# Kernel optimization log

Hardware: AMD Instinct MI355X
Metric: run time of the kernel (lower is better)

## Reference

```python
import jax, jax.numpy as jnp
import numpy as np

B, HH, WW, E = 8, 64, 64, 384
NH, EXP = 6, 2
D1 = (EXP * E) // NH * NH      # 768
HD = D1 // NH                  # 128
RPE = 512
LAYERS = 3
EPS = 1e-6


def srms(x):
    # SimpleRMSNorm: no learnable weight
    return x * jax.lax.rsqrt(jnp.mean(x * x, axis=-1, keepdims=True) + EPS)


def rpe_forward(pos, pw, pb, lw, lb, ow, ob):
    # pos: (n, 1) -> (n, NH*HD). Rpe MLP: act(pos_proj) -> layers x [norm,act,linear] -> out
    x = jax.nn.relu(pos @ pw + pb)
    for i in range(lw.shape[0]):  # fixed small layer count
        x = jax.nn.relu(srms(x)) @ lw[i] + lb[i]
    return jax.nn.relu(srms(x)) @ ow + ob


def tno_coeffs(n, pw, pb, lw, lb, ow, ob):
    # Toeplitz coeffs t_0..t_{n-1}, t_0(dummy), t_{-(n-1)}..t_{-1} for circular conv of len 2n
    pos = jnp.arange(1, n, dtype=jnp.float32)[:, None]             # (n-1, 1), par_type=1
    neg = -jnp.arange(1, n, dtype=jnp.float32)[::-1][:, None]      # -(n-1)..-1
    zero = jnp.zeros((1, 1), dtype=jnp.float32)
    t_zero = rpe_forward(zero, pw, pb, lw, lb, ow, ob)             # (1, NH*HD)
    t_pos = rpe_forward(pos, pw, pb, lw, lb, ow, ob)               # (n-1, NH*HD)
    t_neg = rpe_forward(neg, pw, pb, lw, lb, ow, ob)
    a = jnp.concatenate([t_zero, t_pos, t_zero, t_neg], axis=0)    # (2n, NH*HD)
    return a.reshape(2 * n, NH, HD).transpose(1, 0, 2)             # (NH, 2n, HD)


def tno_apply(v, a, axis):
    # v: (b, h, H, W, d); FFT-based Toeplitz (circular) mixing along `axis` in {-3, -2}
    n = v.shape[axis]
    a = a[:, :, None, :] if axis == -3 else a[:, None, :, :]
    y = jnp.fft.rfft(v, 2 * n, axis=axis)
    af = jnp.fft.rfft(a, 2 * n, axis=axis)
    out = jnp.fft.irfft(af * y, 2 * n, axis=axis)
    return jax.lax.slice_in_dim(out, 0, n, axis=out.ndim + axis)


def setup_inputs() -> dict:
    key = jax.random.key(0)
    ks = jax.random.split(key, 24)
    s = 0.02
    def rn(k, shape):
        return jax.random.normal(k, shape, dtype=jnp.float32) * s
    inp = {
        "x": jax.random.normal(ks[0], (B, HH, WW, E), dtype=jnp.float32),
        "H": HH, "W": WW,
        "Wu": rn(ks[1], (E, D1)), "bu": jnp.zeros((D1,), jnp.float32),
        "Wv": rn(ks[2], (E, D1)), "bv": jnp.zeros((D1,), jnp.float32),
        "Wo": rn(ks[3], (D1, E)), "bo": jnp.zeros((E,), jnp.float32),
    }
    for t, off in (("r1", 4), ("r2", 10)):
        inp[t + "_pw"] = rn(ks[off], (1, RPE))
        inp[t + "_pb"] = jnp.zeros((RPE,), jnp.float32)
        inp[t + "_lw"] = rn(ks[off + 1], (LAYERS, RPE, RPE))
        inp[t + "_lb"] = jnp.zeros((LAYERS, RPE), jnp.float32)
        inp[t + "_ow"] = rn(ks[off + 2], (RPE, NH * HD))
        inp[t + "_ob"] = jnp.zeros((NH * HD,), jnp.float32)
    return inp


def reference(x, H, W, Wu, bu, Wv, bv, Wo, bo,
              r1_pw, r1_pb, r1_lw, r1_lb, r1_ow, r1_ob,
              r2_pw, r2_pb, r2_lw, r2_lb, r2_ow, r2_ob):
    b = x.shape[0]
    xn = srms(x)                                    # pre_norm (SimpleRMSNorm)
    u = jax.nn.silu(xn @ Wu + bu)                   # gate branch
    v = jax.nn.silu(xn @ Wv + bv)
    v = v.reshape(b, H, W, NH, HD).transpose(0, 3, 1, 2, 4)        # b h H W d
    a_h = tno_coeffs(H, r2_pw, r2_pb, r2_lw, r2_lb, r2_ow, r2_ob)  # toep2, dim=-3
    a_w = tno_coeffs(W, r1_pw, r1_pb, r1_lw, r1_lb, r1_ow, r1_ob)  # toep1, dim=-2
    out = tno_apply(v, a_h, -3) + tno_apply(v, a_w, -2)
    out = out.transpose(0, 2, 3, 1, 4).reshape(b, H, W, NH * HD)   # b H W (h d)
    out = u * out
    return out @ Wo + bo + x
```

## Files before the change

### kernel.cpp

```cpp
#include <hip/hip_runtime.h>
#include <stdint.h>


typedef __attribute__((ext_vector_type(4))) float  f32x4;
typedef __attribute__((ext_vector_type(8))) short  s16x8;
typedef __attribute__((ext_vector_type(8))) unsigned short u16x8;
typedef __attribute__((ext_vector_type(4))) unsigned short u16x4;
typedef unsigned short u16;

#define M_TOT 32768
#define E_DIM 384
#define D1    768

__device__ __forceinline__ u16 f2bf(float f) {
  union { float f; unsigned int u; } v; v.f = f;
  unsigned int r = (v.u + 0x7FFFu + ((v.u >> 16) & 1u)) >> 16;
  return (u16)r;
}
__device__ __forceinline__ float bf2f(u16 h) {
  union { unsigned int u; float f; } v; v.u = ((unsigned int)h) << 16;
  return v.f;
}
__device__ __forceinline__ float silu_f(float x) {
  return x * __builtin_amdgcn_rcpf(1.f + __expf(-x));
}

__device__ __forceinline__ void gload_lds16(const u16* g, u16* l) {
  __builtin_amdgcn_global_load_lds(
      (const __attribute__((address_space(1))) uint32_t*)g,
      (__attribute__((address_space(3))) uint32_t*)l, 16, 0, 0);
}

__global__ __launch_bounds__(256) void setup_k(
    const float* __restrict__ x, u16* __restrict__ xn,
    const float* __restrict__ Wu, const float* __restrict__ Wv,
    const float* __restrict__ Wo, u16* __restrict__ Wuvt, u16* __restrict__ Wot,
    const float* __restrict__ r1lw, const float* __restrict__ r1ow,
    const float* __restrict__ r2lw, const float* __restrict__ r2ow,
    u16* __restrict__ lwT, u16* __restrict__ owT,
    const float* __restrict__ r1pw, const float* __restrict__ r1pb,
    const float* __restrict__ r2pw, const float* __restrict__ r2pb,
    float* __restrict__ X0) {
  __shared__ float sm[32][33];
  const int bid = blockIdx.x;
  const int tid = threadIdx.x;

  if (bid < 8192) {
    int row  = bid * 4 + (tid >> 6);
    int lane = tid & 63;
    const float* xr = x + (size_t)row * 384 + lane;
    float v[6]; float ss = 0.f;
#pragma unroll
    for (int i = 0; i < 6; i++) { v[i] = xr[i * 64]; ss += v[i] * v[i]; }
#pragma unroll
    for (int off = 32; off > 0; off >>= 1) ss += __shfl_xor(ss, off);
    float sc = rsqrtf(ss * (1.f / 384.f) + 1e-6f);
    u16* o = xn + (size_t)row * 384 + lane;
#pragma unroll
    for (int i = 0; i < 6; i++) o[i * 64] = f2bf(v[i] * sc);
  } else if (bid < 11360) {
    int b = bid - 8192;
    const float* src; u16* dst; int C, DS, R0, C0;
    if (b < 2304) {
      int mlp = b / 1152, r = b % 1152;
      if (r < 768) {
        int L = r / 256, t = r % 256;
        R0 = (t / 16) * 32; C0 = (t % 16) * 32;
        src = (mlp ? r2lw : r1lw) + (size_t)L * 262144;
        dst = lwT + (size_t)(mlp * 3 + L) * 262144;
        C = 512; DS = 512;
      } else {
        int t = r - 768;
        R0 = (t / 24) * 32; C0 = (t % 24) * 32;
        src = mlp ? r2ow : r1ow;
        dst = owT + (size_t)mlp * 393216;
        C = 768; DS = 512;
      }
    } else {
      int t = b - 2304;
      if (t < 288)      { R0 = (t / 24) * 32; C0 = (t % 24) * 32;
                          src = Wu; C = 768; dst = Wuvt;            DS = 384; }
      else if (t < 576) { int t2 = t - 288; R0 = (t2 / 24) * 32; C0 = (t2 % 24) * 32;
                          src = Wv; C = 768; dst = Wuvt + 768 * 384; DS = 384; }
      else              { int t2 = t - 576; R0 = (t2 / 12) * 32; C0 = (t2 % 12) * 32;
                          src = Wo; C = 384; dst = Wot;             DS = 768; }
    }
    int lx = tid % 32, ly = tid / 32;
#pragma unroll
    for (int q = 0; q < 4; q++) {
      int y = q * 8 + ly;
      sm[y][lx] = src[(size_t)(R0 + y) * C + C0 + lx];
    }
    __syncthreads();
#pragma unroll
    for (int q = 0; q < 4; q++) {
      int y = q * 8 + ly;
      dst[(size_t)(C0 + y) * DS + R0 + lx] = f2bf(sm[lx][y]);
    }
  } else {
    int idx = (bid - 11360) * 256 + tid;
    int gid = idx * 4;
    int row = gid >> 9, col = gid & 511;
    int mlp = row >> 7, p = row & 127;
    float pos = (p < 64) ? (float)p : ((p == 64) ? 0.f : (float)(p - 128));
    const float* pw = (mlp ? r2pw : r1pw) + col;
    const float* pb = (mlp ? r2pb : r1pb) + col;
    f32x4 w = *(const f32x4*)pw;
    f32x4 bb = *(const f32x4*)pb;
    f32x4 o;
#pragma unroll
    for (int e = 0; e < 4; e++) o[e] = fmaxf(pos * w[e] + bb[e], 0.f);
    *(f32x4*)(X0 + gid) = o;
  }
}

template <int N, bool TOUT>
__global__ __launch_bounds__(256) void rpe_layer_k(
    const float* __restrict__ X,
    const u16* __restrict__ wtA, const u16* __restrict__ wtB,
    const float* __restrict__ bA, const float* __restrict__ bB,
    float* __restrict__ outA, float* __restrict__ outB) {
  constexpr int NT = N / 128;
  const int mlp = blockIdx.x / NT;
  const int n0  = (blockIdx.x % NT) * 128;
  const u16* WT = mlp ? wtB : wtA;
  const float* bias = mlp ? bB : bA;
  float* out = mlp ? outB : outA;
  const float* Xm = X + (size_t)mlp * 128 * 512;

  __shared__ float scale[128];
  __shared__ __align__(16) u16 As[128 * 64];
  __shared__ __align__(16) u16 Bs[128 * 64];

  const int tid  = threadIdx.x;
  const int lane = tid & 63;
  const int wid  = tid >> 6;
  const int wm   = wid >> 1, wn = wid & 1;
  const int fl   = lane & 15, fh = lane >> 4;

  {
    int row = tid >> 1, half = tid & 1;
    const float* xr = Xm + (size_t)row * 512 + half * 256;
    float ss = 0.f;
#pragma unroll 8
    for (int q = 0; q < 64; q++) {
      f32x4 v = *(const f32x4*)(xr + q * 4);
      ss += v[0] * v[0] + v[1] * v[1] + v[2] * v[2] + v[3] * v[3];
    }
    ss += __shfl_xor(ss, 1);
    if (!half) scale[row] = rsqrtf(ss * (1.f / 512.f) + 1e-6f);
  }
  __syncthreads();

  f32x4 acc[4][4];
  {
    f32x4 z = {0.f, 0.f, 0.f, 0.f};
#pragma unroll
    for (int i = 0; i < 4; i++)
#pragma unroll
      for (int j = 0; j < 4; j++) acc[i][j] = z;
  }

  const int arow = tid >> 1, acb = (tid & 1) * 32;
  const int sr = tid >> 3, sc = (tid & 7) * 8;

  for (int kt = 0; kt < 512; kt += 64) {
    {
      const float* xp = Xm + (size_t)arow * 512 + kt + acb;
      float s_ = scale[arow];
      u16* dst = As + arow * 64 + acb;
#pragma unroll
      for (int q = 0; q < 8; q++) {
        f32x4 v = *(const f32x4*)(xp + q * 4);
        u16x4 pk;
#pragma unroll
        for (int e = 0; e < 4; e++) pk[e] = f2bf(fmaxf(v[e], 0.f) * s_);
        *(u16x4*)(dst + q * 4) = pk;
      }
    }
    {
      const u16* gB = WT + (size_t)(n0 + sr) * 512 + kt + sc;
      u16* lB = Bs + sr * 64 + sc;
#pragma unroll
      for (int i = 0; i < 4; i++)
        gload_lds16(gB + (size_t)(i * 32) * 512, lB + i * 32 * 64);
    }
    __syncthreads();
#pragma unroll
    for (int ks = 0; ks < 2; ks++) {
      s16x8 af[4], bfr[4];
      const u16* ap = As + (wm * 64 + fl) * 64 + ks * 32 + fh * 8;
      const u16* bp = Bs + (wn * 64 + fl) * 64 + ks * 32 + fh * 8;
#pragma unroll
      for (int i = 0; i < 4; i++) af[i] = *(const s16x8*)(ap + i * 16 * 64);
#pragma unroll
      for (int j = 0; j < 4; j++) bfr[j] = *(const s16x8*)(bp + j * 16 * 64);
#pragma unroll
      for (int i = 0; i < 4; i++)
#pragma unroll
        for (int j = 0; j < 4; j++)
          acc[i][j] = __builtin_amdgcn_mfma_f32_16x16x32_bf16(af[i], bfr[j], acc[i][j], 0, 0, 0);
    }
    __syncthreads();
  }

#pragma unroll
  for (int i = 0; i < 4; i++)
#pragma unroll
    for (int j = 0; j < 4; j++) {
      int c = n0 + wn * 64 + j * 16 + fl;
      float bv_ = bias[c];
#pragma unroll
      for (int q = 0; q < 4; q++) {
        int r = wm * 64 + i * 16 + fh * 4 + q;
        if (TOUT) out[(size_t)c * 128 + r] = acc[i][j][q] + bv_;
        else      out[(size_t)r * N + c]   = acc[i][j][q] + bv_;
      }
    }
}

template <int MODE>
__global__ __launch_bounds__(256) void gemm_k(
    const u16* __restrict__ A, const u16* __restrict__ Bt, int K,
    u16* __restrict__ u_out, u16* __restrict__ vt_out,
    const float* __restrict__ bu, const float* __restrict__ bv,
    float* __restrict__ out, const float* __restrict__ bo,
    const float* __restrict__ xres) {
  __shared__ __align__(16) char smem[34816];
  u16*   As  = (u16*)smem;
  u16*   Bs  = As + 128 * 64;
  float* epi = (float*)smem;

  const int tid  = threadIdx.x;
  const int lane = tid & 63;
  const int wid  = tid >> 6;
  const int wm   = wid >> 1, wn = wid & 1;
  const int bm   = blockIdx.x & 255, bn = blockIdx.x >> 8;
  const int m0   = bm * 128, n0 = bn * 128;
  const int fl   = lane & 15, fh = lane >> 4;

  f32x4 acc[4][4];
  {
    f32x4 z = {0.f, 0.f, 0.f, 0.f};
#pragma unroll
    for (int i = 0; i < 4; i++)
#pragma unroll
      for (int j = 0; j < 4; j++) acc[i][j] = z;
  }

  const int sr  = tid >> 3;
  const int scl = (tid & 7) * 8;
  const int scs = ((tid & 7) ^ (sr & 7)) * 8;
  const int cr  = tid & 63;
  const int mw  = ((tid >> 6) & 3) * 32;

  for (int kt = 0; kt < K; kt += 64) {
    if (MODE == 1) {
      const u16* ga = A + (size_t)(kt + cr) * M_TOT + m0 + mw;
      u16x8 rr[4];
      rr[0] = *(const u16x8*)(ga);
      rr[1] = *(const u16x8*)(ga + 8);
      rr[2] = *(const u16x8*)(ga + 16);
      rr[3] = *(const u16x8*)(ga + 24);
      const int cb8 = cr >> 3, off = cr & 7;
#pragma unroll
      for (int v = 0; v < 4; v++)
#pragma unroll
        for (int e = 0; e < 8; e++)
          As[(mw + v * 8 + e) * 64 + ((cb8 ^ e) << 3) + off] = rr[v][e];
    } else {
      const u16* gA = A + (size_t)(m0 + sr) * K + kt + scs;
      u16* lA = As + sr * 64 + scl;
#pragma unroll
      for (int i = 0; i < 4; i++)
        gload_lds16(gA + (size_t)(i * 32) * K, lA + i * 32 * 64);
    }
    {
      const u16* gB = Bt + (size_t)(n0 + sr) * K + kt + scs;
      u16* lB = Bs + sr * 64 + scl;
#pragma unroll
      for (int i = 0; i < 4; i++)
        gload_lds16(gB + (size_t)(i * 32) * K, lB + i * 32 * 64);
    }
    __syncthreads();
#pragma unroll
    for (int ks = 0; ks < 2; ks++) {
      s16x8 af[4], bfr[4];
      const int xc = ((ks * 4 + fh) ^ (fl & 7)) * 8;
      const u16* ap = As + (wm * 64 + fl) * 64 + xc;
      const u16* bp = Bs + (wn * 64 + fl) * 64 + xc;
#pragma unroll
      for (int i = 0; i < 4; i++) af[i] = *(const s16x8*)(ap + i * 16 * 64);
#pragma unroll
      for (int j = 0; j < 4; j++) bfr[j] = *(const s16x8*)(bp + j * 16 * 64);
#pragma unroll
      for (int i = 0; i < 4; i++)
#pragma unroll
        for (int j = 0; j < 4; j++)
          acc[i][j] = __builtin_amdgcn_mfma_f32_16x16x32_bf16(af[i], bfr[j], acc[i][j], 0, 0, 0);
    }
    __syncthreads();
  }

  for (int half = 0; half < 2; half++) {
    __syncthreads();
    if (wm == half) {
#pragma unroll
      for (int i = 0; i < 4; i++)
#pragma unroll
        for (int j = 0; j < 4; j++) {
          int er = i * 16 + fh * 4;
          int ec = wn * 64 + j * 16 + fl;
#pragma unroll
          for (int q = 0; q < 4; q++) epi[(er + q) * 132 + ec] = acc[i][j][q];
        }
    }
    __syncthreads();
    if (MODE == 0) {
      const bool isU = (n0 < 768);
      u16* baseo = isU ? u_out : vt_out;
      const int cc = tid >> 1;
      const int cg = (isU ? n0 : n0 - 768) + cc;
      const float bias_v = (isU ? bu : bv)[cg];
      u16* dst = baseo + (size_t)cg * M_TOT + m0 + half * 64;
#pragma unroll
      for (int q = 0; q < 4; q++) {
        int mb = (tid & 1) * 8 + q * 16;
        u16x8 pk;
#pragma unroll
        for (int e = 0; e < 8; e++) {
          int mm = mb + e;
          pk[e] = f2bf(silu_f(epi[mm * 132 + cc] + bias_v));
        }
        *(u16x8*)(dst + mb) = pk;
      }
    } else {
      int rr = tid >> 2;
      int gm = m0 + half * 64 + rr;
      const float* xr = xres + (size_t)gm * 384 + n0;
      float* orow = out + (size_t)gm * 384 + n0;
#pragma unroll
      for (int q = 0; q < 8; q++) {
        int cb = (tid & 3) * 4 + q * 16;
        f32x4 xv = *(const f32x4*)(xr + cb);
        f32x4 ov;
#pragma unroll
        for (int e = 0; e < 4; e++) {
          int c = cb + e;
          ov[e] = epi[rr * 132 + c] + bo[n0 + c] + xv[e];
        }
        *(f32x4*)(orow + cb) = ov;
      }
    }
  }
}

__global__ __launch_bounds__(256) void conv_k(const u16* __restrict__ vt,
                                              const u16* __restrict__ ut,
                                              const float* __restrict__ a_hT,
                                              const float* __restrict__ a_wT,
                                              u16* __restrict__ gT) {
  __shared__ __align__(16) char smraw[5 * 64 * 72 * 2 + 1024];
  u16* Vs  = (u16*)smraw;
  u16* VTs = Vs + 64 * 72;
  u16* Ths = VTs + 64 * 72;
  u16* Tws = Ths + 64 * 72;
  u16* Us  = Tws + 64 * 72;
  float* ahs = (float*)(Us + 64 * 72);
  float* aws = ahs + 128;
  u16* epi = Ths;

  const int tid = threadIdx.x;
  const int c = blockIdx.x >> 3, b = blockIdx.x & 7;
  const u16* srcv = vt + (size_t)c * M_TOT + b * 4096;
  const u16* srcu = ut + (size_t)c * M_TOT + b * 4096;

  {
    int y = tid >> 2, x0 = (tid & 3) * 16;
    *(u16x8*)(Vs + y * 72 + x0)     = *(const u16x8*)(srcv + y * 64 + x0);
    *(u16x8*)(Vs + y * 72 + x0 + 8) = *(const u16x8*)(srcv + y * 64 + x0 + 8);
    *(u16x8*)(Us + y * 72 + x0)     = *(const u16x8*)(srcu + y * 64 + x0);
    *(u16x8*)(Us + y * 72 + x0 + 8) = *(const u16x8*)(srcu + y * 64 + x0 + 8);
  }
  if (tid < 128) ahs[tid] = a_hT[(size_t)c * 128 + tid];
  else           aws[tid - 128] = a_wT[(size_t)c * 128 + (tid - 128)];
  __syncthreads();

  {
    int y = tid & 63, j0 = (tid >> 6) * 16;
#pragma unroll
    for (int e = 0; e < 16; e++) {
      int j = j0 + e;
      VTs[j * 72 + y] = Vs[y * 72 + j];
      Ths[y * 72 + j] = f2bf(ahs[(y - j) & 127]);
      Tws[y * 72 + j] = f2bf(aws[(y - j) & 127]);
    }
  }
  __syncthreads();

  const int lane = tid & 63, w = tid >> 6;
  const int fl = lane & 15, fh = lane >> 4;
  f32x4 acc[4];
  {
    f32x4 z = {0.f, 0.f, 0.f, 0.f};
#pragma unroll
    for (int i = 0; i < 4; i++) acc[i] = z;
  }

#pragma unroll
  for (int ks = 0; ks < 2; ks++) {
    s16x8 qh = *(const s16x8*)(Ths + (w * 16 + fl) * 72 + ks * 32 + fh * 8);
#pragma unroll
    for (int i = 0; i < 4; i++) {
      s16x8 p = *(const s16x8*)(VTs + (i * 16 + fl) * 72 + ks * 32 + fh * 8);
      acc[i] = __builtin_amdgcn_mfma_f32_16x16x32_bf16(p, qh, acc[i], 0, 0, 0);
    }
    s16x8 qw = *(const s16x8*)(Vs + (w * 16 + fl) * 72 + ks * 32 + fh * 8);
#pragma unroll
    for (int i = 0; i < 4; i++) {
      s16x8 p = *(const s16x8*)(Tws + (i * 16 + fl) * 72 + ks * 32 + fh * 8);
      acc[i] = __builtin_amdgcn_mfma_f32_16x16x32_bf16(p, qw, acc[i], 0, 0, 0);
    }
  }
  __syncthreads();

  {
    int y = w * 16 + fl;
#pragma unroll
    for (int i = 0; i < 4; i++) {
      u16x4 pk;
#pragma unroll
      for (int e = 0; e < 4; e++) {
        int xx = i * 16 + fh * 4 + e;
        pk[e] = f2bf(acc[i][e] * bf2f(Us[y * 72 + xx]));
      }
      *(u16x4*)(epi + y * 72 + i * 16 + fh * 4) = pk;
    }
  }
  __syncthreads();

  {
    int y = tid >> 2, x0 = (tid & 3) * 16;
    u16x8 a0 = *(const u16x8*)(epi + y * 72 + x0);
    u16x8 a1 = *(const u16x8*)(epi + y * 72 + x0 + 8);
    u16* dst = gT + (size_t)c * M_TOT + b * 4096 + y * 64 + x0;
    *(u16x8*)dst = a0;
    *(u16x8*)(dst + 8) = a1;
  }
}

extern "C" void kernel_launch(void* const* d_in, const int* in_sizes, int n_in,
                              void* d_out, int out_size, void* d_ws, size_t ws_size,
                              hipStream_t stream) {
  const float* x    = (const float*)d_in[0];
  const float* Wu   = (const float*)d_in[3];
  const float* bu   = (const float*)d_in[4];
  const float* Wv   = (const float*)d_in[5];
  const float* bv   = (const float*)d_in[6];
  const float* Wo   = (const float*)d_in[7];
  const float* bo   = (const float*)d_in[8];
  const float* r1pw = (const float*)d_in[9];
  const float* r1pb = (const float*)d_in[10];
  const float* r1lw = (const float*)d_in[11];
  const float* r1lb = (const float*)d_in[12];
  const float* r1ow = (const float*)d_in[13];
  const float* r1ob = (const float*)d_in[14];
  const float* r2pw = (const float*)d_in[15];
  const float* r2pb = (const float*)d_in[16];
  const float* r2lw = (const float*)d_in[17];
  const float* r2lb = (const float*)d_in[18];
  const float* r2ow = (const float*)d_in[19];
  const float* r2ob = (const float*)d_in[20];
  float* outp = (float*)d_out;

  char* ws = (char*)d_ws;
  size_t off = 0;
  auto carve = [&](size_t bytes) {
    char* p = ws + off;
    off += (bytes + 255) & ~(size_t)255;
    return p;
  };
  u16*   xn   = (u16*)carve((size_t)M_TOT * 384 * 2);
  u16*   uT   = (u16*)carve((size_t)768 * M_TOT * 2);
  u16*   vT   = (u16*)carve((size_t)768 * M_TOT * 2);
  u16*   gT   = (u16*)carve((size_t)768 * M_TOT * 2);
  u16*   Wuvt = (u16*)carve((size_t)1536 * 384 * 2);
  u16*   Wot  = (u16*)carve((size_t)384 * 768 * 2);
  float* awT  = (float*)carve((size_t)768 * 128 * 4);
  float* ahT  = (float*)carve((size_t)768 * 128 * 4);

  char* rb  = (char*)gT;
  u16*   lwT = (u16*)rb;
  u16*   owT = (u16*)(rb + 3145728);
  float* X0  = (float*)(rb + 3145728 + 1572864);
  float* X1  = X0 + 256 * 512;

  setup_k<<<11488, 256, 0, stream>>>(x, xn, Wu, Wv, Wo, Wuvt, Wot,
                                     r1lw, r1ow, r2lw, r2ow, lwT, owT,
                                     r1pw, r1pb, r2pw, r2pb, X0);

  rpe_layer_k<512, false><<<8, 256, 0, stream>>>(X0, lwT, lwT + 3 * 262144,
                                                 r1lb, r2lb, X1, X1 + 128 * 512);
  rpe_layer_k<512, false><<<8, 256, 0, stream>>>(X1, lwT + 262144, lwT + 4 * 262144,
                                                 r1lb + 512, r2lb + 512, X0, X0 + 128 * 512);
  rpe_layer_k<512, false><<<8, 256, 0, stream>>>(X0, lwT + 2 * 262144, lwT + 5 * 262144,
                                                 r1lb + 1024, r2lb + 1024, X1, X1 + 128 * 512);
  rpe_layer_k<768, true><<<12, 256, 0, stream>>>(X1, owT, owT + 393216,
                                                 r1ob, r2ob, awT, ahT);

  gemm_k<0><<<256 * 12, 256, 0, stream>>>(xn, Wuvt, 384,
                                          uT, vT, bu, bv,
                                          nullptr, nullptr, nullptr);
  conv_k<<<768 * 8, 256, 0, stream>>>(vT, uT, ahT, awT, gT);
  gemm_k<1><<<256 * 3, 256, 0, stream>>>(gT, Wot, 768,
                                         nullptr, nullptr, nullptr, nullptr,
                                         outp, bo, x);
}
```

Measured before the change: 432.4 us.

## Split GEMM kernels, widen output GEMM tile, loop batches in conv kernel

Result: faster. 395.9 us (-8.4%).

```diff
diff --git a/kernel.cpp b/kernel.cpp
--- a/kernel.cpp
+++ b/kernel.cpp
@@ -9,8 +9,6 @@
 typedef unsigned short u16;
 
 #define M_TOT 32768
-#define E_DIM 384
-#define D1    768
 
 __device__ __forceinline__ u16 f2bf(float f) {
   union { float f; unsigned int u; } v; v.f = f;
@@ -79,11 +77,11 @@
     } else {
       int t = b - 2304;
       if (t < 288)      { R0 = (t / 24) * 32; C0 = (t % 24) * 32;
-                          src = Wu; C = 768; dst = Wuvt;            DS = 384; }
+                          src = Wu; C = 768; dst = Wuvt;             DS = 384; }
       else if (t < 576) { int t2 = t - 288; R0 = (t2 / 24) * 32; C0 = (t2 % 24) * 32;
                           src = Wv; C = 768; dst = Wuvt + 768 * 384; DS = 384; }
       else              { int t2 = t - 576; R0 = (t2 / 12) * 32; C0 = (t2 % 12) * 32;
-                          src = Wo; C = 384; dst = Wot;             DS = 768; }
+                          src = Wo; C = 384; dst = Wot;              DS = 768; }
     }
     int lx = tid % 32, ly = tid / 32;
 #pragma unroll
@@ -219,13 +217,10 @@
     }
 }
 
-template <int MODE>
-__global__ __launch_bounds__(256) void gemm_k(
-    const u16* __restrict__ A, const u16* __restrict__ Bt, int K,
+__global__ __launch_bounds__(256) void gemm0_k(
+    const u16* __restrict__ A, const u16* __restrict__ Bt,
     u16* __restrict__ u_out, u16* __restrict__ vt_out,
-    const float* __restrict__ bu, const float* __restrict__ bv,
-    float* __restrict__ out, const float* __restrict__ bo,
-    const float* __restrict__ xres) {
+    const float* __restrict__ bu, const float* __restrict__ bv) {
   __shared__ __align__(16) char smem[34816];
   u16*   As  = (u16*)smem;
   u16*   Bs  = As + 128 * 64;
@@ -238,6 +233,7 @@
   const int bm   = blockIdx.x & 255, bn = blockIdx.x >> 8;
   const int m0   = bm * 128, n0 = bn * 128;
   const int fl   = lane & 15, fh = lane >> 4;
+  const int K    = 384;
 
   f32x4 acc[4][4];
   {
@@ -251,36 +247,16 @@
   const int sr  = tid >> 3;
   const int scl = (tid & 7) * 8;
   const int scs = ((tid & 7) ^ (sr & 7)) * 8;
-  const int cr  = tid & 63;
-  const int mw  = ((tid >> 6) & 3) * 32;
 
   for (int kt = 0; kt < K; kt += 64) {
-    if (MODE == 1) {
-      const u16* ga = A + (size_t)(kt + cr) * M_TOT + m0 + mw;
-      u16x8 rr[4];
-      rr[0] = *(const u16x8*)(ga);
-      rr[1] = *(const u16x8*)(ga + 8);
-      rr[2] = *(const u16x8*)(ga + 16);
-      rr[3] = *(const u16x8*)(ga + 24);
-      const int cb8 = cr >> 3, off = cr & 7;
-#pragma unroll
-      for (int v = 0; v < 4; v++)
-#pragma unroll
-        for (int e = 0; e < 8; e++)
-          As[(mw + v * 8 + e) * 64 + ((cb8 ^ e) << 3) + off] = rr[v][e];
-    } else {
-      const u16* gA = A + (size_t)(m0 + sr) * K + kt + scs;
-      u16* lA = As + sr * 64 + scl;
-#pragma unroll
-      for (int i = 0; i < 4; i++)
-        gload_lds16(gA + (size_t)(i * 32) * K, lA + i * 32 * 64);
-    }
-    {
-      const u16* gB = Bt + (size_t)(n0 + sr) * K + kt + scs;
-      u16* lB = Bs + sr * 64 + scl;
-#pragma unroll
-      for (int i = 0; i < 4; i++)
-        gload_lds16(gB + (size_t)(i * 32) * K, lB + i * 32 * 64);
+    const u16* gA = A  + (size_t)(m0 + sr) * K + kt + scs;
+    const u16* gB = Bt + (size_t)(n0 + sr) * K + kt + scs;
+    u16* lA = As + sr * 64 + scl;
+    u16* lB = Bs + sr * 64 + scl;
+#pragma unroll
+    for (int i = 0; i < 4; i++) {
+      gload_lds16(gA + (size_t)(i * 32) * K, lA + i * 32 * 64);
+      gload_lds16(gB + (size_t)(i * 32) * K, lB + i * 32 * 64);
     }
     __syncthreads();
 #pragma unroll
@@ -316,40 +292,107 @@
         }
     }
     __syncthreads();
-    if (MODE == 0) {
-      const bool isU = (n0 < 768);
-      u16* baseo = isU ? u_out : vt_out;
-      const int cc = tid >> 1;
-      const int cg = (isU ? n0 : n0 - 768) + cc;
-      const float bias_v = (isU ? bu : bv)[cg];
-      u16* dst = baseo + (size_t)cg * M_TOT + m0 + half * 64;
-#pragma unroll
-      for (int q = 0; q < 4; q++) {
-        int mb = (tid & 1) * 8 + q * 16;
-        u16x8 pk;
-#pragma unroll
-        for (int e = 0; e < 8; e++) {
-          int mm = mb + e;
-          pk[e] = f2bf(silu_f(epi[mm * 132 + cc] + bias_v));
-        }
-        *(u16x8*)(dst + mb) = pk;
-      }
-    } else {
-      int rr = tid >> 2;
-      int gm = m0 + half * 64 + rr;
-      const float* xr = xres + (size_t)gm * 384 + n0;
-      float* orow = out + (size_t)gm * 384 + n0;
-#pragma unroll
-      for (int q = 0; q < 8; q++) {
-        int cb = (tid & 3) * 4 + q * 16;
-        f32x4 xv = *(const f32x4*)(xr + cb);
-        f32x4 ov;
-#pragma unroll
-        for (int e = 0; e < 4; e++) {
-          int c = cb + e;
-          ov[e] = epi[rr * 132 + c] + bo[n0 + c] + xv[e];
-        }
-        *(f32x4*)(orow + cb) = ov;
+    const bool isU = (n0 < 768);
+    u16* baseo = isU ? u_out : vt_out;
+    const int cc = tid >> 1;
+    const int cg = (isU ? n0 : n0 - 768) + cc;
+    const float bias_v = (isU ? bu : bv)[cg];
+    u16* dst = baseo + (size_t)cg * M_TOT + m0 + half * 64;
+#pragma unroll
+    for (int q = 0; q < 4; q++) {
+      int mb = (tid & 1) * 8 + q * 16;
+      u16x8 pk;
+#pragma unroll
+      for (int e = 0; e < 8; e++) {
+        int mm = mb + e;
+        pk[e] = f2bf(silu_f(epi[mm * 132 + cc] + bias_v));
+      }
+      *(u16x8*)(dst + mb) = pk;
+    }
+  }
+}
+
+__global__ __launch_bounds__(512, 2) void gemm2_k(
+    const u16* __restrict__ gT, const u16* __restrict__ Wot,
+    float* __restrict__ out, const float* __restrict__ bo,
+    const float* __restrict__ xres) {
+  __shared__ __align__(16) u16 As[128 * 64];
+  __shared__ __align__(16) u16 Bs[384 * 64];
+
+  const int tid  = threadIdx.x;
+  const int lane = tid & 63;
+  const int wid  = tid >> 6;
+  const int wm   = wid >> 2;
+  const int wn   = wid & 3;
+  const int m0   = blockIdx.x * 128;
+  const int fl   = lane & 15, fh = lane >> 4;
+
+  f32x4 acc[4][6];
+  {
+    f32x4 z = {0.f, 0.f, 0.f, 0.f};
+#pragma unroll
+    for (int i = 0; i < 4; i++)
+#pragma unroll
+      for (int j = 0; j < 6; j++) acc[i][j] = z;
+  }
+
+  const int sr  = tid >> 3;
+  const int scl = (tid & 7) * 8;
+  const int scs = ((tid & 7) ^ (sr & 7)) * 8;
+  const int cr  = tid & 63;
+  const int mw  = (tid >> 6) * 16;
+  const int c8  = cr >> 3, of = cr & 7;
+
+  for (int kt = 0; kt < 768; kt += 64) {
+#pragma unroll
+    for (int i = 0; i < 6; i++)
+      gload_lds16(Wot + (size_t)(sr + 64 * i) * 768 + kt + scs,
+                  Bs + (sr + 64 * i) * 64 + scl);
+    {
+      const u16* ga = gT + (size_t)(kt + cr) * M_TOT + m0 + mw;
+      u16x8 r0 = *(const u16x8*)ga;
+      u16x8 r1 = *(const u16x8*)(ga + 8);
+#pragma unroll
+      for (int e = 0; e < 8; e++)
+        As[(mw + e) * 64 + ((c8 ^ e) << 3) + of] = r0[e];
+#pragma unroll
+      for (int e = 0; e < 8; e++)
+        As[(mw + 8 + e) * 64 + ((c8 ^ e) << 3) + of] = r1[e];
+    }
+    __syncthreads();
+#pragma unroll
+    for (int ks = 0; ks < 2; ks++) {
+      s16x8 af[4], bfr[6];
+      const int xc = ((ks * 4 + fh) ^ (fl & 7)) * 8;
+      const u16* ap = As + (wm * 64 + fl) * 64 + xc;
+      const u16* bp = Bs + (wn * 96 + fl) * 64 + xc;
+#pragma unroll
+      for (int i = 0; i < 4; i++) af[i] = *(const s16x8*)(ap + i * 16 * 64);
+#pragma unroll
+      for (int j = 0; j < 6; j++) bfr[j] = *(const s16x8*)(bp + j * 16 * 64);
+#pragma unroll
+      for (int i = 0; i < 4; i++)
+#pragma unroll
+        for (int j = 0; j < 6; j++)
+          acc[i][j] = __builtin_amdgcn_mfma_f32_16x16x32_bf16(af[i], bfr[j], acc[i][j], 0, 0, 0);
+    }
+    __syncthreads();
+  }
+
+  float bov[6];
+#pragma unroll
+  for (int j = 0; j < 6; j++) bov[j] = bo[wn * 96 + j * 16 + fl];
+#pragma unroll
+  for (int i = 0; i < 4; i++) {
+#pragma unroll
+    for (int q = 0; q < 4; q++) {
+      int m = m0 + wm * 64 + i * 16 + fh * 4 + q;
+      const float* xr = xres + (size_t)m * 384;
+      float* orow = out + (size_t)m * 384;
+#pragma unroll
+      for (int j = 0; j < 6; j++) {
+        int n = wn * 96 + j * 16 + fl;
+        orow[n] = acc[i][j][q] + bov[j] + xr[n];
       }
     }
   }
@@ -360,92 +403,110 @@
                                               const float* __restrict__ a_hT,
                                               const float* __restrict__ a_wT,
                                               u16* __restrict__ gT) {
-  __shared__ __align__(16) char smraw[5 * 64 * 72 * 2 + 1024];
-  u16* Vs  = (u16*)smraw;
-  u16* VTs = Vs + 64 * 72;
-  u16* Ths = VTs + 64 * 72;
-  u16* Tws = Ths + 64 * 72;
-  u16* Us  = Tws + 64 * 72;
-  float* ahs = (float*)(Us + 64 * 72);
-  float* aws = ahs + 128;
-  u16* epi = Ths;
+  __shared__ __align__(16) u16 Th[64 * 72];
+  __shared__ __align__(16) u16 Tw[64 * 72];
+  __shared__ __align__(16) u16 Vs[64 * 72];
+  __shared__ __align__(16) u16 VTs[64 * 72];
+  __shared__ __align__(16) u16 Us[64 * 72];
+  __shared__ float ahr[192];
+  __shared__ float awr[192];
+  u16* epi = VTs;
 
   const int tid = threadIdx.x;
-  const int c = blockIdx.x >> 3, b = blockIdx.x & 7;
-  const u16* srcv = vt + (size_t)c * M_TOT + b * 4096;
-  const u16* srcu = ut + (size_t)c * M_TOT + b * 4096;
-
-  {
-    int y = tid >> 2, x0 = (tid & 3) * 16;
-    *(u16x8*)(Vs + y * 72 + x0)     = *(const u16x8*)(srcv + y * 64 + x0);
-    *(u16x8*)(Vs + y * 72 + x0 + 8) = *(const u16x8*)(srcv + y * 64 + x0 + 8);
-    *(u16x8*)(Us + y * 72 + x0)     = *(const u16x8*)(srcu + y * 64 + x0);
-    *(u16x8*)(Us + y * 72 + x0 + 8) = *(const u16x8*)(srcu + y * 64 + x0 + 8);
-  }
-  if (tid < 128) ahs[tid] = a_hT[(size_t)c * 128 + tid];
-  else           aws[tid - 128] = a_wT[(size_t)c * 128 + (tid - 128)];
+  const int c = blockIdx.x;
+  const int lane = tid & 63, w = tid >> 6;
+  const int fl = lane & 15, fh = lane >> 4;
+
+  if (tid < 192) {
+    int idx = (128 - tid) & 127;
+    ahr[tid] = a_hT[(size_t)c * 128 + idx];
+    awr[tid] = a_wT[(size_t)c * 128 + idx];
+  }
   __syncthreads();
 
   {
     int y = tid & 63, j0 = (tid >> 6) * 16;
-#pragma unroll
-    for (int e = 0; e < 16; e++) {
-      int j = j0 + e;
-      VTs[j * 72 + y] = Vs[y * 72 + j];
-      Ths[y * 72 + j] = f2bf(ahs[(y - j) & 127]);
-      Tws[y * 72 + j] = f2bf(aws[(y - j) & 127]);
-    }
-  }
-  __syncthreads();
-
-  const int lane = tid & 63, w = tid >> 6;
-  const int fl = lane & 15, fh = lane >> 4;
-  f32x4 acc[4];
-  {
-    f32x4 z = {0.f, 0.f, 0.f, 0.f};
-#pragma unroll
-    for (int i = 0; i < 4; i++) acc[i] = z;
-  }
-
-#pragma unroll
-  for (int ks = 0; ks < 2; ks++) {
-    s16x8 qh = *(const s16x8*)(Ths + (w * 16 + fl) * 72 + ks * 32 + fh * 8);
-#pragma unroll
-    for (int i = 0; i < 4; i++) {
-      s16x8 p = *(const s16x8*)(VTs + (i * 16 + fl) * 72 + ks * 32 + fh * 8);
-      acc[i] = __builtin_amdgcn_mfma_f32_16x16x32_bf16(p, qh, acc[i], 0, 0, 0);
-    }
-    s16x8 qw = *(const s16x8*)(Vs + (w * 16 + fl) * 72 + ks * 32 + fh * 8);
-#pragma unroll
-    for (int i = 0; i < 4; i++) {
-      s16x8 p = *(const s16x8*)(Tws + (i * 16 + fl) * 72 + ks * 32 + fh * 8);
-      acc[i] = __builtin_amdgcn_mfma_f32_16x16x32_bf16(p, qw, acc[i], 0, 0, 0);
-    }
-  }
-  __syncthreads();
-
-  {
-    int y = w * 16 + fl;
-#pragma unroll
-    for (int i = 0; i < 4; i++) {
-      u16x4 pk;
-#pragma unroll
-      for (int e = 0; e < 4; e++) {
-        int xx = i * 16 + fh * 4 + e;
-        pk[e] = f2bf(acc[i][e] * bf2f(Us[y * 72 + xx]));
-      }
-      *(u16x4*)(epi + y * 72 + i * 16 + fh * 4) = pk;
-    }
-  }
-  __syncthreads();
-
-  {
-    int y = tid >> 2, x0 = (tid & 3) * 16;
-    u16x8 a0 = *(const u16x8*)(epi + y * 72 + x0);
-    u16x8 a1 = *(const u16x8*)(epi + y * 72 + x0 + 8);
-    u16* dst = gT + (size_t)c * M_TOT + b * 4096 + y * 64 + x0;
-    *(u16x8*)dst = a0;
-    *(u16x8*)(dst + 8) = a1;
+    int base = 128 - y + j0;
+    u16x8 p0, p1, q0, q1;
+#pragma unroll
+    for (int e = 0; e < 8; e++) {
+      p0[e] = f2bf(ahr[base + e]);
+      p1[e] = f2bf(ahr[base + 8 + e]);
+      q0[e] = f2bf(awr[base + e]);
+      q1[e] = f2bf(awr[base + 8 + e]);
+    }
+    *(u16x8*)(Th + y * 72 + j0)     = p0;
+    *(u16x8*)(Th + y * 72 + j0 + 8) = p1;
+    *(u16x8*)(Tw + y * 72 + j0)     = q0;
+    *(u16x8*)(Tw + y * 72 + j0 + 8) = q1;
+  }
+
+  const int sy = tid >> 2, sx = (tid & 3) * 16;
+  const int ty = tid & 63, tj = (tid >> 6) * 16;
+
+  for (int b = 0; b < 8; b++) {
+    const u16* srcv = vt + (size_t)c * M_TOT + b * 4096;
+    const u16* srcu = ut + (size_t)c * M_TOT + b * 4096;
+    *(u16x8*)(Vs + sy * 72 + sx)     = *(const u16x8*)(srcv + sy * 64 + sx);
+    *(u16x8*)(Vs + sy * 72 + sx + 8) = *(const u16x8*)(srcv + sy * 64 + sx + 8);
+    *(u16x8*)(Us + sy * 72 + sx)     = *(const u16x8*)(srcu + sy * 64 + sx);
+    *(u16x8*)(Us + sy * 72 + sx + 8) = *(const u16x8*)(srcu + sy * 64 + sx + 8);
+    __syncthreads();
+
+    {
+      u16x8 q0 = *(const u16x8*)(Vs + ty * 72 + tj);
+      u16x8 q1 = *(const u16x8*)(Vs + ty * 72 + tj + 8);
+#pragma unroll
+      for (int e = 0; e < 8; e++) VTs[(tj + e) * 72 + ty]     = q0[e];
+#pragma unroll
+      for (int e = 0; e < 8; e++) VTs[(tj + 8 + e) * 72 + ty] = q1[e];
+    }
+    __syncthreads();
+
+    f32x4 acc[4];
+    {
+      f32x4 z = {0.f, 0.f, 0.f, 0.f};
+#pragma unroll
+      for (int i = 0; i < 4; i++) acc[i] = z;
+    }
+#pragma unroll
+    for (int ks = 0; ks < 2; ks++) {
+      s16x8 qh = *(const s16x8*)(Th + (w * 16 + fl) * 72 + ks * 32 + fh * 8);
+#pragma unroll
+      for (int i = 0; i < 4; i++) {
+        s16x8 p = *(const s16x8*)(VTs + (i * 16 + fl) * 72 + ks * 32 + fh * 8);
+        acc[i] = __builtin_amdgcn_mfma_f32_16x16x32_bf16(p, qh, acc[i], 0, 0, 0);
+      }
+      s16x8 qw = *(const s16x8*)(Vs + (w * 16 + fl) * 72 + ks * 32 + fh * 8);
+#pragma unroll
+      for (int i = 0; i < 4; i++) {
+        s16x8 p = *(const s16x8*)(Tw + (i * 16 + fl) * 72 + ks * 32 + fh * 8);
+        acc[i] = __builtin_amdgcn_mfma_f32_16x16x32_bf16(p, qw, acc[i], 0, 0, 0);
+      }
+    }
+    __syncthreads();
+
+    {
+      int y = w * 16 + fl;
+#pragma unroll
+      for (int i = 0; i < 4; i++) {
+        u16x4 uq = *(const u16x4*)(Us + y * 72 + i * 16 + fh * 4);
+        u16x4 pk;
+#pragma unroll
+        for (int e = 0; e < 4; e++) pk[e] = f2bf(acc[i][e] * bf2f(uq[e]));
+        *(u16x4*)(epi + y * 72 + i * 16 + fh * 4) = pk;
+      }
+    }
+    __syncthreads();
+
+    {
+      u16x8 a0 = *(const u16x8*)(epi + sy * 72 + sx);
+      u16x8 a1 = *(const u16x8*)(epi + sy * 72 + sx + 8);
+      u16* dst = gT + (size_t)c * M_TOT + b * 4096 + sy * 64 + sx;
+      *(u16x8*)dst = a0;
+      *(u16x8*)(dst + 8) = a1;
+    }
+    __syncthreads();
   }
 }
 
@@ -508,11 +569,7 @@
   rpe_layer_k<768, true><<<12, 256, 0, stream>>>(X1, owT, owT + 393216,
                                                  r1ob, r2ob, awT, ahT);
 
-  gemm_k<0><<<256 * 12, 256, 0, stream>>>(xn, Wuvt, 384,
-                                          uT, vT, bu, bv,
-                                          nullptr, nullptr, nullptr);
-  conv_k<<<768 * 8, 256, 0, stream>>>(vT, uT, ahT, awT, gT);
-  gemm_k<1><<<256 * 3, 256, 0, stream>>>(gT, Wot, 768,
-                                         nullptr, nullptr, nullptr, nullptr,
-                                         outp, bo, x);
-}
+  gemm0_k<<<256 * 12, 256, 0, stream>>>(xn, Wuvt, uT, vT, bu, bv);
+  conv_k<<<768, 256, 0, stream>>>(vT, uT, ahT, awT, gT);
+  gemm2_k<<<256, 512, 0, stream>>>(gT, Wot, outp, bo, x);
+}
```
